# Kernel tuning notes

Measured on AMD Instinct MI355X. Metric: run time of the kernel, lower is better.

## Reference

```python
import jax, jax.numpy as jnp
import numpy as np

KH, KW = 5, 5  # hardcoded in the module's build()


def setup_inputs() -> dict:
    key = jax.random.key(0)
    k1, k2 = jax.random.split(key)
    # inputs are cast to int32 inside call(); use integer-valued floats so the
    # cast is meaningful (pixel-like values in [0, 256)).
    inputs = jax.random.randint(k1, (4, 224, 224, 16), 0, 256).astype(jnp.float32)
    # learned kernel, shape (5, 5, C_in, filters); small signed integer values
    kernel = jax.random.randint(k2, (5, 5, 16, 32), -8, 8).astype(jnp.float32)
    return {"inputs": inputs, "kernel": kernel}


def reference(inputs, kernel):
    # Faithful int32 math: cast inputs and kernel to int32 as in call().
    x = inputs.astype(jnp.int32)            # [B, H, W, C]
    k = kernel.astype(jnp.int32)            # [KH, KW, C, F]
    B, H, W, C = x.shape
    F = k.shape[-1]
    Ho, Wo = H - KH + 1, W - KW + 1         # VALID 2D cross-correlation
    # Per-(channel, filter) conv with NO reduction over channels: fuse the
    # C_in*F separate MyConv2D launches into one vectorized 25-tap accumulation.
    out = jnp.zeros((B, Ho, Wo, C, F), dtype=jnp.int32)
    for i in range(KH):
        for j in range(KW):
            out = out + x[:, i:i + Ho, j:j + Wo, :, None] * k[i, j, :, :]
    # tf.stack(filters, axis=2) then tf.stack(channels, axis=2) produces
    # output layout [B, Ho, C, F, Wo].
    out = jnp.transpose(out, (0, 1, 3, 4, 2))
    return out.astype(jnp.float32)
```

## Files before the change

kernel.cpp:

```cpp
#include <hip/hip_runtime.h>

#define KH 5
#define KW 5
#define CIN 16
#define NF 32
#define H 224
#define W 224
#define HO 220
#define WO 220

__global__ __launch_bounds__(256) void conv2d_perchan_kernel(
    const float* __restrict__ X,
    const float* __restrict__ Kw,
    float* __restrict__ O)
{
    __shared__ float xs[KH * W];
    __shared__ float ws[KH * KW * NF];

    const int c  = blockIdx.x;
    const int ho = blockIdx.y;
    const int b  = blockIdx.z;
    const int t  = threadIdx.x;

    const float* xbase = X + ((size_t)(b * H + ho) * W) * CIN + c;
    for (int idx = t; idx < KH * W; idx += 256) {
        xs[idx] = xbase[(size_t)idx * CIN];
    }
    for (int idx = t; idx < KH * KW * NF; idx += 256) {
        const int tap = idx >> 5;
        const int f   = idx & 31;
        ws[idx] = Kw[(size_t)tap * (CIN * NF) + c * NF + f];
    }
    __syncthreads();

    const int wave = t >> 6;
    const int lane = t & 63;
    const int f0   = wave * 8;
    const int wo0  = lane * 4;
    if (lane >= 55) return;

    float acc[8][4];
#pragma unroll
    for (int f = 0; f < 8; ++f)
#pragma unroll
        for (int r = 0; r < 4; ++r) acc[f][r] = 0.0f;

#pragma unroll
    for (int i = 0; i < KH; ++i) {
        const float4 xa = *(const float4*)&xs[i * W + wo0];
        const float4 xb = *(const float4*)&xs[i * W + wo0 + 4];
        float xr[8] = {xa.x, xa.y, xa.z, xa.w, xb.x, xb.y, xb.z, xb.w};
#pragma unroll
        for (int j = 0; j < KW; ++j) {
            const float4 w0 = *(const float4*)&ws[(i * KW + j) * NF + f0];
            const float4 w1 = *(const float4*)&ws[(i * KW + j) * NF + f0 + 4];
            const float wv[8] = {w0.x, w0.y, w0.z, w0.w, w1.x, w1.y, w1.z, w1.w};
#pragma unroll
            for (int f = 0; f < 8; ++f)
#pragma unroll
                for (int r = 0; r < 4; ++r)
                    acc[f][r] += xr[j + r] * wv[f];
        }
    }

    const size_t obase = (((size_t)(b * HO + ho) * CIN + c) * NF + f0) * WO + wo0;
#pragma unroll
    for (int f = 0; f < 8; ++f) {
        *(float4*)&O[obase + (size_t)f * WO] =
            make_float4(acc[f][0], acc[f][1], acc[f][2], acc[f][3]);
    }
}

extern "C" void kernel_launch(void* const* d_in, const int* in_sizes, int n_in,
                              void* d_out, int out_size, void* d_ws, size_t ws_size,
                              hipStream_t stream) {
    const float* X  = (const float*)d_in[0];
    const float* Kw = (const float*)d_in[1];
    float* O        = (float*)d_out;

    dim3 grid(CIN, HO, 4);
    conv2d_perchan_kernel<<<grid, 256, 0, stream>>>(X, Kw, O);
}
```

Baseline: 463.2 us.

## Load weights as wave-uniform scalars and loop over filters with register-held input rows

Drops the shared-memory weight buffer and instead reads each filter's 25 taps straight from global memory, using readfirstlane so they become wave-uniform scalar loads. Each thread keeps all five input rows in registers and loops over its 8 filters one at a time, writing each output row as it finishes. This removes the LDS weight reads and shrinks the accumulator set from 32 to 4 registers, which should raise occupancy. In exchange it issues more scalar global loads per block, and the kernel stays bound by output-store bandwidth.

```diff
diff --git a/kernel.cpp b/kernel.cpp
--- a/kernel.cpp
+++ b/kernel.cpp
@@ -15,7 +15,6 @@
     float* __restrict__ O)
 {
     __shared__ float xs[KH * W];
-    __shared__ float ws[KH * KW * NF];
 
     const int c  = blockIdx.x;
     const int ho = blockIdx.y;
@@ -26,48 +25,46 @@
     for (int idx = t; idx < KH * W; idx += 256) {
         xs[idx] = xbase[(size_t)idx * CIN];
     }
-    for (int idx = t; idx < KH * KW * NF; idx += 256) {
-        const int tap = idx >> 5;
-        const int f   = idx & 31;
-        ws[idx] = Kw[(size_t)tap * (CIN * NF) + c * NF + f];
-    }
     __syncthreads();
 
     const int wave = t >> 6;
     const int lane = t & 63;
-    const int f0   = wave * 8;
     const int wo0  = lane * 4;
     if (lane >= 55) return;
 
-    float acc[8][4];
-#pragma unroll
-    for (int f = 0; f < 8; ++f)
-#pragma unroll
-        for (int r = 0; r < 4; ++r) acc[f][r] = 0.0f;
-
+    float xr[KH][8];
 #pragma unroll
     for (int i = 0; i < KH; ++i) {
         const float4 xa = *(const float4*)&xs[i * W + wo0];
         const float4 xb = *(const float4*)&xs[i * W + wo0 + 4];
-        float xr[8] = {xa.x, xa.y, xa.z, xa.w, xb.x, xb.y, xb.z, xb.w};
-#pragma unroll
-        for (int j = 0; j < KW; ++j) {
-            const float4 w0 = *(const float4*)&ws[(i * KW + j) * NF + f0];
-            const float4 w1 = *(const float4*)&ws[(i * KW + j) * NF + f0 + 4];
-            const float wv[8] = {w0.x, w0.y, w0.z, w0.w, w1.x, w1.y, w1.z, w1.w};
-#pragma unroll
-            for (int f = 0; f < 8; ++f)
-#pragma unroll
-                for (int r = 0; r < 4; ++r)
-                    acc[f][r] += xr[j + r] * wv[f];
-        }
+        xr[i][0] = xa.x; xr[i][1] = xa.y; xr[i][2] = xa.z; xr[i][3] = xa.w;
+        xr[i][4] = xb.x; xr[i][5] = xb.y; xr[i][6] = xb.z; xr[i][7] = xb.w;
     }
 
-    const size_t obase = (((size_t)(b * HO + ho) * CIN + c) * NF + f0) * WO + wo0;
+    const float* kwc = Kw + c * NF;
+    const size_t orow = (((size_t)(b * HO + ho) * CIN + c) * NF) * WO + wo0;
+
+#pragma unroll 2
+    for (int fi = 0; fi < 8; ++fi) {
+        const int f = __builtin_amdgcn_readfirstlane(wave * 8 + fi);
+        float wk[KH * KW];
 #pragma unroll
-    for (int f = 0; f < 8; ++f) {
-        *(float4*)&O[obase + (size_t)f * WO] =
-            make_float4(acc[f][0], acc[f][1], acc[f][2], acc[f][3]);
+        for (int tap = 0; tap < KH * KW; ++tap)
+            wk[tap] = kwc[(size_t)tap * (CIN * NF) + f];
+
+        float acc0 = 0.f, acc1 = 0.f, acc2 = 0.f, acc3 = 0.f;
+#pragma unroll
+        for (int i = 0; i < KH; ++i)
+#pragma unroll
+            for (int j = 0; j < KW; ++j) {
+                const float w = wk[i * KW + j];
+                acc0 += xr[i][j + 0] * w;
+                acc1 += xr[i][j + 1] * w;
+                acc2 += xr[i][j + 2] * w;
+                acc3 += xr[i][j + 3] * w;
+            }
+
+        *(float4*)&O[orow + (size_t)f * WO] = make_float4(acc0, acc1, acc2, acc3);
     }
 }
 
```

New measurement: 454.0 us. -2.0%, faster.
